# Optimization experiments

Hardware: AMD Instinct MI355X
Metric: run time of the kernel (lower is better)

## Reference

```python
import jax, jax.numpy as jnp
import numpy as np

EPS_LEN = 1e-20
EPS_DENOM = 1e-6


def _dot(a, b):
    return jnp.sum(a * b, axis=-1, keepdims=True)


def _safe_normalize(x):
    return x / jnp.sqrt(jnp.maximum(_dot(x, x), EPS_LEN))


def _auto_normals(positions, faces):
    i0, i1, i2 = faces[:, 0], faces[:, 1], faces[:, 2]
    v0 = positions[i0]
    v1 = positions[i1]
    v2 = positions[i2]
    face_normals = jnp.cross(v1 - v0, v2 - v0)  # [F,3]
    v_nrm = jnp.zeros_like(positions)
    v_nrm = v_nrm.at[i0].add(face_normals)
    v_nrm = v_nrm.at[i1].add(face_normals)
    v_nrm = v_nrm.at[i2].add(face_normals)
    default = jnp.array([0.0, 0.0, 1.0], dtype=positions.dtype)
    v_nrm = jnp.where(_dot(v_nrm, v_nrm) > EPS_LEN, v_nrm, default)
    return _safe_normalize(v_nrm)


def _compute_tangents(positions, normals, faces, texcoords, uv_faces):
    pos = [positions[faces[:, i]] for i in range(3)]
    tex = [texcoords[uv_faces[:, i]] for i in range(3)]
    uve1 = tex[1] - tex[0]
    uve2 = tex[2] - tex[0]
    pe1 = pos[1] - pos[0]
    pe2 = pos[2] - pos[0]
    nom = pe1 * uve2[..., 1:2] - pe2 * uve1[..., 1:2]  # [F,3]
    denom = uve1[..., 0:1] * uve2[..., 1:2] - uve1[..., 1:2] * uve2[..., 0:1]
    denom = jnp.where(denom > 0.0,
                      jnp.maximum(denom, EPS_DENOM),
                      jnp.minimum(denom, -EPS_DENOM))
    tang = nom / denom  # [F,3]
    tangents = jnp.zeros_like(normals)
    for i in range(3):
        tangents = tangents.at[faces[:, i]].add(tang)
    tangents = _safe_normalize(tangents)
    tangents = _safe_normalize(tangents - _dot(tangents, normals) * normals)
    return tangents


def setup_inputs() -> dict:
    key = jax.random.key(0)
    k1, k2, k3, k4 = jax.random.split(key, 4)
    V, T, F = 2_000_000, 2_200_000, 4_000_000
    positions = jax.random.normal(k1, (V, 3), dtype=jnp.float32)
    faces = jax.random.randint(k2, (F, 3), 0, V, dtype=jnp.int32)
    texcoords = jax.random.uniform(k3, (T, 2), dtype=jnp.float32)
    uv_faces = jax.random.randint(k4, (F, 3), 0, T, dtype=jnp.int32)
    return {"positions": positions, "faces": faces,
            "texcoords": texcoords, "uv_faces": uv_faces}


def reference(positions, faces, texcoords, uv_faces):
    normals = _auto_normals(positions, faces)
    tangents = _compute_tangents(positions, normals, faces, texcoords, uv_faces)
    return jnp.stack([normals, tangents])  # [2, V, 3]
```

## Files before the change

### kernel.cpp

```cpp
#include <hip/hip_runtime.h>

#define EPS_LEN   1e-20f
#define EPS_DENOM 1e-6f

#define CB_LOG   13
#define CB       (1 << CB_LOG)
#define QLOG     11
#define QSIZE    (1 << QLOG)
#define CAP_C    57344
#define FST      6
#define BLKA     1024
#define MAXB     256

__global__ __launch_bounds__(BLKA)
void vg_face_bin(const float* __restrict__ pos, const int* __restrict__ faces,
                 const float* __restrict__ tex, const int* __restrict__ uvf,
                 float* __restrict__ face_data,
                 unsigned* __restrict__ ef, unsigned short* __restrict__ ev,
                 int* __restrict__ cursors, int* __restrict__ validw,
                 float* __restrict__ nacc, float* __restrict__ tacc,
                 int F, int NBC)
{
    __shared__ int h[MAXB], sc[MAXB], loff[MAXB], lfill[MAXB], gbase[MAXB];
    __shared__ unsigned       sface[3 * BLKA];
    __shared__ unsigned short svloc[3 * BLKA];
    __shared__ unsigned char  sbuck[3 * BLKA];

    const int t = threadIdx.x;
    const int f = blockIdx.x * BLKA + t;

    if (t < MAXB) { h[t] = 0; lfill[t] = 0; }
    for (int i = t; i < 3 * BLKA; i += BLKA) sbuck[i] = 0xFF;
    __syncthreads();

    const bool on = (f < F);
    int i0 = 0, i1 = 0, i2 = 0;
    float nx = 0, ny = 0, nz = 0, txv = 0, tyv = 0, tzv = 0;

    if (on) {
        i0 = faces[3 * f + 0]; i1 = faces[3 * f + 1]; i2 = faces[3 * f + 2];

        const float p0x = pos[3*i0+0], p0y = pos[3*i0+1], p0z = pos[3*i0+2];
        const float p1x = pos[3*i1+0], p1y = pos[3*i1+1], p1z = pos[3*i1+2];
        const float p2x = pos[3*i2+0], p2y = pos[3*i2+1], p2z = pos[3*i2+2];

        const float e1x = p1x - p0x, e1y = p1y - p0y, e1z = p1z - p0z;
        const float e2x = p2x - p0x, e2y = p2y - p0y, e2z = p2z - p0z;

        nx = e1y * e2z - e1z * e2y;
        ny = e1z * e2x - e1x * e2z;
        nz = e1x * e2y - e1y * e2x;

        const int t0 = uvf[3 * f + 0];
        const int t1 = uvf[3 * f + 1];
        const int t2 = uvf[3 * f + 2];

        const float u0x = tex[2*t0+0], u0y = tex[2*t0+1];
        const float u1x = tex[2*t1+0], u1y = tex[2*t1+1];
        const float u2x = tex[2*t2+0], u2y = tex[2*t2+1];

        const float d1x = u1x - u0x, d1y = u1y - u0y;
        const float d2x = u2x - u0x, d2y = u2y - u0y;

        float denom = d1x * d2y - d1y * d2x;
        denom = (denom > 0.0f) ? fmaxf(denom, EPS_DENOM) : fminf(denom, -EPS_DENOM);
        const float inv = 1.0f / denom;

        txv = (e1x * d2y - e2x * d1y) * inv;
        tyv = (e1y * d2y - e2y * d1y) * inv;
        tzv = (e1z * d2y - e2z * d1y) * inv;

        float* fd = &face_data[(size_t)f * FST];
        reinterpret_cast<float2*>(fd)[0] = make_float2(nx, ny);
        reinterpret_cast<float2*>(fd)[1] = make_float2(nz, txv);
        reinterpret_cast<float2*>(fd)[2] = make_float2(tyv, tzv);

        atomicAdd(&h[i0 >> CB_LOG], 1);
        atomicAdd(&h[i1 >> CB_LOG], 1);
        atomicAdd(&h[i2 >> CB_LOG], 1);
    }
    __syncthreads();

    if (t < MAXB) sc[t] = h[t];
    __syncthreads();
    for (int d = 1; d < MAXB; d <<= 1) {
        int v2 = 0;
        if (t < MAXB) v2 = sc[t] + ((t >= d) ? sc[t - d] : 0);
        __syncthreads();
        if (t < MAXB) sc[t] = v2;
        __syncthreads();
    }
    if (t < MAXB) {
        loff[t] = sc[t] - h[t];
        const int cnt = h[t];
        int gb = -1;
        if (t < NBC && cnt > 0) {
            gb = atomicAdd(&cursors[t], cnt);
            if (gb + cnt <= CAP_C) atomicMax(&validw[t], gb + cnt);
            else gb = -1;
        }
        gbase[t] = gb;
    }
    __syncthreads();

    if (on) {
        const int vi[3] = { i0, i1, i2 };
#pragma unroll
        for (int c = 0; c < 3; ++c) {
            const int v = vi[c];
            const int b = v >> CB_LOG;
            if (gbase[b] >= 0) {
                const int slot = atomicAdd(&lfill[b], 1);
                const int p = loff[b] + slot;
                sface[p] = (unsigned)f;
                svloc[p] = (unsigned short)(v & (CB - 1));
                sbuck[p] = (unsigned char)b;
            } else {
                atomicAdd(&nacc[3*v+0], nx);
                atomicAdd(&nacc[3*v+1], ny);
                atomicAdd(&nacc[3*v+2], nz);
                atomicAdd(&tacc[3*v+0], txv);
                atomicAdd(&tacc[3*v+1], tyv);
                atomicAdd(&tacc[3*v+2], tzv);
            }
        }
    }
    __syncthreads();

    for (int i = t; i < 3 * BLKA; i += BLKA) {
        const unsigned b = sbuck[i];
        if (b != 0xFFu) {
            const int g = gbase[b] + (i - loff[b]);
            const size_t base = (size_t)b * CAP_C;
            ef[base + g] = sface[i];
            ev[base + g] = svloc[i];
        }
    }
}

__global__ __launch_bounds__(BLKA)
void vg_bucket_reduce(const float* __restrict__ face_data,
                      const unsigned* __restrict__ ef,
                      const unsigned short* __restrict__ ev,
                      const int* __restrict__ validw,
                      float* __restrict__ nacc, float* __restrict__ tacc,
                      int V)
{
    __shared__ float acc[QSIZE * 6];
    const int b = blockIdx.x;
    const int t = threadIdx.x;
    int count = validw[b];
    if (count > CAP_C) count = CAP_C;
    const size_t ebase = (size_t)b * CAP_C;
    const int vbase = b << CB_LOG;

    for (int q = 0; q < 4; ++q) {
        for (int i = t; i < QSIZE * 6; i += BLKA) acc[i] = 0.0f;
        __syncthreads();

        for (int e = t; e < count; e += BLKA) {
            const int vloc = (int)ev[ebase + e];
            if ((vloc >> QLOG) == q) {
                const unsigned f = ef[ebase + e];
                const float* fd = &face_data[(size_t)f * FST];
                const float2 a0 = reinterpret_cast<const float2*>(fd)[0];
                const float2 a1 = reinterpret_cast<const float2*>(fd)[1];
                const float2 a2 = reinterpret_cast<const float2*>(fd)[2];
                float* a = &acc[(vloc & (QSIZE - 1)) * 6];
                atomicAdd(a + 0, a0.x);
                atomicAdd(a + 1, a0.y);
                atomicAdd(a + 2, a1.x);
                atomicAdd(a + 3, a1.y);
                atomicAdd(a + 4, a2.x);
                atomicAdd(a + 5, a2.y);
            }
        }
        __syncthreads();

        for (int i = t; i < QSIZE; i += BLKA) {
            const int v = vbase + (q << QLOG) + i;
            if (v < V) {
                float nx = nacc[3*v+0] + acc[i*6+0];
                float ny = nacc[3*v+1] + acc[i*6+1];
                float nz = nacc[3*v+2] + acc[i*6+2];
                float tx = tacc[3*v+0] + acc[i*6+3];
                float ty = tacc[3*v+1] + acc[i*6+4];
                float tz = tacc[3*v+2] + acc[i*6+5];

                const float nd = nx*nx + ny*ny + nz*nz;
                if (nd > EPS_LEN) {
                    const float invn = 1.0f / sqrtf(nd);
                    nx *= invn; ny *= invn; nz *= invn;
                } else {
                    nx = 0.0f; ny = 0.0f; nz = 1.0f;
                }

                const float td = tx*tx + ty*ty + tz*tz;
                const float invt = 1.0f / sqrtf(fmaxf(td, EPS_LEN));
                tx *= invt; ty *= invt; tz *= invt;

                const float dp = tx*nx + ty*ny + tz*nz;
                tx -= dp * nx; ty -= dp * ny; tz -= dp * nz;

                const float td2 = tx*tx + ty*ty + tz*tz;
                const float invt2 = 1.0f / sqrtf(fmaxf(td2, EPS_LEN));
                tx *= invt2; ty *= invt2; tz *= invt2;

                nacc[3*v+0] = nx; nacc[3*v+1] = ny; nacc[3*v+2] = nz;
                tacc[3*v+0] = tx; tacc[3*v+1] = ty; tacc[3*v+2] = tz;
            }
        }
        __syncthreads();
    }
}

__global__ void vg_face_kernel(const float* __restrict__ pos,
                               const int*   __restrict__ faces,
                               const float* __restrict__ tex,
                               const int*   __restrict__ uvf,
                               float* __restrict__ nacc,
                               float* __restrict__ tacc,
                               int F) {
    int f = blockIdx.x * blockDim.x + threadIdx.x;
    if (f >= F) return;

    const int i0 = faces[3*f+0], i1 = faces[3*f+1], i2 = faces[3*f+2];

    const float p0x = pos[3*i0+0], p0y = pos[3*i0+1], p0z = pos[3*i0+2];
    const float p1x = pos[3*i1+0], p1y = pos[3*i1+1], p1z = pos[3*i1+2];
    const float p2x = pos[3*i2+0], p2y = pos[3*i2+1], p2z = pos[3*i2+2];

    const float e1x = p1x - p0x, e1y = p1y - p0y, e1z = p1z - p0z;
    const float e2x = p2x - p0x, e2y = p2y - p0y, e2z = p2z - p0z;

    const float nx = e1y*e2z - e1z*e2y;
    const float ny = e1z*e2x - e1x*e2z;
    const float nz = e1x*e2y - e1y*e2x;

    const int t0 = uvf[3*f+0], t1 = uvf[3*f+1], t2 = uvf[3*f+2];

    const float u0x = tex[2*t0+0], u0y = tex[2*t0+1];
    const float u1x = tex[2*t1+0], u1y = tex[2*t1+1];
    const float u2x = tex[2*t2+0], u2y = tex[2*t2+1];

    const float d1x = u1x - u0x, d1y = u1y - u0y;
    const float d2x = u2x - u0x, d2y = u2y - u0y;

    float denom = d1x * d2y - d1y * d2x;
    denom = (denom > 0.0f) ? fmaxf(denom, EPS_DENOM) : fminf(denom, -EPS_DENOM);
    const float inv = 1.0f / denom;

    const float tx = (e1x*d2y - e2x*d1y) * inv;
    const float ty = (e1y*d2y - e2y*d1y) * inv;
    const float tz = (e1z*d2y - e2z*d1y) * inv;

    atomicAdd(&nacc[3*i0+0], nx); atomicAdd(&nacc[3*i0+1], ny); atomicAdd(&nacc[3*i0+2], nz);
    atomicAdd(&nacc[3*i1+0], nx); atomicAdd(&nacc[3*i1+1], ny); atomicAdd(&nacc[3*i1+2], nz);
    atomicAdd(&nacc[3*i2+0], nx); atomicAdd(&nacc[3*i2+1], ny); atomicAdd(&nacc[3*i2+2], nz);
    atomicAdd(&tacc[3*i0+0], tx); atomicAdd(&tacc[3*i0+1], ty); atomicAdd(&tacc[3*i0+2], tz);
    atomicAdd(&tacc[3*i1+0], tx); atomicAdd(&tacc[3*i1+1], ty); atomicAdd(&tacc[3*i1+2], tz);
    atomicAdd(&tacc[3*i2+0], tx); atomicAdd(&tacc[3*i2+1], ty); atomicAdd(&tacc[3*i2+2], tz);
}

__global__ void vg_finalize_kernel(float* __restrict__ nacc,
                                   float* __restrict__ tacc,
                                   int V) {
    int v = blockIdx.x * blockDim.x + threadIdx.x;
    if (v >= V) return;

    float nx = nacc[3*v+0], ny = nacc[3*v+1], nz = nacc[3*v+2];
    float nd = nx*nx + ny*ny + nz*nz;
    if (nd > EPS_LEN) {
        const float invn = 1.0f / sqrtf(nd);
        nx *= invn; ny *= invn; nz *= invn;
    } else {
        nx = 0.0f; ny = 0.0f; nz = 1.0f;
    }

    float tx = tacc[3*v+0], ty = tacc[3*v+1], tz = tacc[3*v+2];
    float td = tx*tx + ty*ty + tz*tz;
    float invt = 1.0f / sqrtf(fmaxf(td, EPS_LEN));
    tx *= invt; ty *= invt; tz *= invt;
    const float dp = tx*nx + ty*ny + tz*nz;
    tx -= dp*nx; ty -= dp*ny; tz -= dp*nz;
    float td2 = tx*tx + ty*ty + tz*tz;
    float invt2 = 1.0f / sqrtf(fmaxf(td2, EPS_LEN));
    tx *= invt2; ty *= invt2; tz *= invt2;

    nacc[3*v+0] = nx; nacc[3*v+1] = ny; nacc[3*v+2] = nz;
    tacc[3*v+0] = tx; tacc[3*v+1] = ty; tacc[3*v+2] = tz;
}

extern "C" void kernel_launch(void* const* d_in, const int* in_sizes, int n_in,
                              void* d_out, int out_size, void* d_ws, size_t ws_size,
                              hipStream_t stream) {
    const float* pos   = (const float*)d_in[0];
    const int*   faces = (const int*)  d_in[1];
    const float* tex   = (const float*)d_in[2];
    const int*   uvf   = (const int*)  d_in[3];

    const int V = in_sizes[0] / 3;
    const int F = in_sizes[1] / 3;

    float* out  = (float*)d_out;
    float* nacc = out;
    float* tacc = out + (size_t)3 * V;

    const int NBC = (V + CB - 1) >> CB_LOG;

    const size_t face_bytes = ((size_t)F * FST * sizeof(float) + 255) & ~(size_t)255;
    const size_t ef_bytes   = ((size_t)NBC * CAP_C * sizeof(unsigned) + 255) & ~(size_t)255;
    const size_t ev_bytes   = ((size_t)NBC * CAP_C * sizeof(unsigned short) + 255) & ~(size_t)255;
    const size_t cur_bytes  = (size_t)NBC * sizeof(int);
    const size_t need = face_bytes + ef_bytes + ev_bytes + 2 * cur_bytes + 256;

    hipMemsetAsync(d_out, 0, (size_t)out_size * sizeof(float), stream);

    if (ws_size < need || NBC > 255 || F >= (1 << 22)) {
        const int BLK = 256;
        vg_face_kernel<<<(F + BLK - 1) / BLK, BLK, 0, stream>>>(pos, faces, tex, uvf,
                                                                nacc, tacc, F);
        vg_finalize_kernel<<<(V + BLK - 1) / BLK, BLK, 0, stream>>>(nacc, tacc, V);
        return;
    }

    char* ws = (char*)d_ws;
    float*          face_data = (float*)ws;
    unsigned*       ef        = (unsigned*)(ws + face_bytes);
    unsigned short* ev        = (unsigned short*)(ws + face_bytes + ef_bytes);
    int*            cursors   = (int*)(ws + face_bytes + ef_bytes + ev_bytes);
    int*            validw    = cursors + NBC;

    hipMemsetAsync(cursors, 0, 2 * cur_bytes, stream);

    vg_face_bin<<<(F + BLKA - 1) / BLKA, BLKA, 0, stream>>>(
        pos, faces, tex, uvf, face_data, ef, ev, cursors, validw, nacc, tacc, F, NBC);

    vg_bucket_reduce<<<NBC, BLKA, 0, stream>>>(
        face_data, ef, ev, validw, nacc, tacc, V);
}
```

Baseline: 937.3 us.

## Bin face payloads directly per vertex bucket instead of face indices

The binning kernel now writes the face normal and tangent values straight into per-bucket payload arrays, in place of a face index that the reduce kernel then uses for a random gather from face_data. The new reduce kernel streams those payloads sequentially and accumulates a whole 8192-vertex bucket in shared memory in one pass, finalizing normals and then tangents. The goal is to replace scattered gathers and the four-pass quarter loop with coalesced reads. In exchange, binned entries grow from 6 to 26 bytes each, so workspace use and write traffic rise, and the per-bucket capacity shrinks, sending more overflow entries to global atomics.

```diff
diff --git a/kernel.cpp b/kernel.cpp
--- a/kernel.cpp
+++ b/kernel.cpp
@@ -5,24 +5,28 @@
 
 #define CB_LOG   13
 #define CB       (1 << CB_LOG)
+#define BLKA     1024
+#define MAXB     256
+#define CAP1     50176
+#define CAP2     57344
+#define FST      6
 #define QLOG     11
 #define QSIZE    (1 << QLOG)
-#define CAP_C    57344
-#define FST      6
-#define BLKA     1024
-#define MAXB     256
+#define VPT      (CB / BLKA)
 
 __global__ __launch_bounds__(BLKA)
-void vg_face_bin(const float* __restrict__ pos, const int* __restrict__ faces,
-                 const float* __restrict__ tex, const int* __restrict__ uvf,
-                 float* __restrict__ face_data,
-                 unsigned* __restrict__ ef, unsigned short* __restrict__ ev,
-                 int* __restrict__ cursors, int* __restrict__ validw,
-                 float* __restrict__ nacc, float* __restrict__ tacc,
-                 int F, int NBC)
+void vg_face_bin_pay(const float* __restrict__ pos, const int* __restrict__ faces,
+                     const float* __restrict__ tex, const int* __restrict__ uvf,
+                     float* __restrict__ en, float* __restrict__ et,
+                     unsigned short* __restrict__ ev,
+                     int* __restrict__ cursors, int* __restrict__ validw,
+                     float* __restrict__ nacc, float* __restrict__ tacc,
+                     int F, int NBC)
 {
     __shared__ int h[MAXB], sc[MAXB], loff[MAXB], lfill[MAXB], gbase[MAXB];
-    __shared__ unsigned       sface[3 * BLKA];
+    __shared__ float spnx[BLKA], spny[BLKA], spnz[BLKA];
+    __shared__ float sptx[BLKA], spty[BLKA], sptz[BLKA];
+    __shared__ unsigned short sfl[3 * BLKA];
     __shared__ unsigned short svloc[3 * BLKA];
     __shared__ unsigned char  sbuck[3 * BLKA];
 
@@ -70,10 +74,8 @@
         tyv = (e1y * d2y - e2y * d1y) * inv;
         tzv = (e1z * d2y - e2z * d1y) * inv;
 
-        float* fd = &face_data[(size_t)f * FST];
-        reinterpret_cast<float2*>(fd)[0] = make_float2(nx, ny);
-        reinterpret_cast<float2*>(fd)[1] = make_float2(nz, txv);
-        reinterpret_cast<float2*>(fd)[2] = make_float2(tyv, tzv);
+        spnx[t] = nx;  spny[t] = ny;  spnz[t] = nz;
+        sptx[t] = txv; spty[t] = tyv; sptz[t] = tzv;
 
         atomicAdd(&h[i0 >> CB_LOG], 1);
         atomicAdd(&h[i1 >> CB_LOG], 1);
@@ -96,7 +98,228 @@
         int gb = -1;
         if (t < NBC && cnt > 0) {
             gb = atomicAdd(&cursors[t], cnt);
-            if (gb + cnt <= CAP_C) atomicMax(&validw[t], gb + cnt);
+            if (gb + cnt <= CAP1) atomicMax(&validw[t], gb + cnt);
+            else gb = -1;
+        }
+        gbase[t] = gb;
+    }
+    __syncthreads();
+
+    if (on) {
+        const int vi[3] = { i0, i1, i2 };
+#pragma unroll
+        for (int c = 0; c < 3; ++c) {
+            const int v = vi[c];
+            const int b = v >> CB_LOG;
+            if (gbase[b] >= 0) {
+                const int slot = atomicAdd(&lfill[b], 1);
+                const int p = loff[b] + slot;
+                sfl[p]   = (unsigned short)t;
+                svloc[p] = (unsigned short)(v & (CB - 1));
+                sbuck[p] = (unsigned char)b;
+            } else {
+                atomicAdd(&nacc[3*v+0], nx);
+                atomicAdd(&nacc[3*v+1], ny);
+                atomicAdd(&nacc[3*v+2], nz);
+                atomicAdd(&tacc[3*v+0], txv);
+                atomicAdd(&tacc[3*v+1], tyv);
+                atomicAdd(&tacc[3*v+2], tzv);
+            }
+        }
+    }
+    __syncthreads();
+
+    for (int i = t; i < 3 * BLKA; i += BLKA) {
+        const unsigned b = sbuck[i];
+        if (b != 0xFFu) {
+            const int g = gbase[b] + (i - loff[b]);
+            const size_t s = (size_t)b * CAP1 + g;
+            const int fl = sfl[i];
+            float* pn = &en[s * 3];
+            pn[0] = spnx[fl]; pn[1] = spny[fl]; pn[2] = spnz[fl];
+            float* pt = &et[s * 3];
+            pt[0] = sptx[fl]; pt[1] = spty[fl]; pt[2] = sptz[fl];
+            ev[s] = svloc[i];
+        }
+    }
+}
+
+__global__ __launch_bounds__(BLKA)
+void vg_reduce_pay(const float* __restrict__ en, const float* __restrict__ et,
+                   const unsigned short* __restrict__ ev,
+                   const int* __restrict__ validw,
+                   float* __restrict__ nacc, float* __restrict__ tacc,
+                   int V)
+{
+    __shared__ float acc[CB * 3];
+    const int b = blockIdx.x;
+    const int t = threadIdx.x;
+    int count = validw[b];
+    if (count > CAP1) count = CAP1;
+    const size_t ebase = (size_t)b * CAP1;
+    const int vbase = b << CB_LOG;
+
+    float nreg[VPT][3];
+
+    for (int i = t; i < CB * 3; i += BLKA) acc[i] = 0.0f;
+    __syncthreads();
+
+    for (int e = t; e < count; e += BLKA) {
+        const int vloc = (int)ev[ebase + e];
+        const float* p = &en[(ebase + e) * 3];
+        float* a = &acc[vloc * 3];
+        atomicAdd(a + 0, p[0]);
+        atomicAdd(a + 1, p[1]);
+        atomicAdd(a + 2, p[2]);
+    }
+    __syncthreads();
+
+#pragma unroll
+    for (int k = 0; k < VPT; ++k) {
+        const int i = t + k * BLKA;
+        const int v = vbase + i;
+        float nx = 0.0f, ny = 0.0f, nz = 1.0f;
+        if (v < V) {
+            nx = nacc[3*v+0] + acc[3*i+0];
+            ny = nacc[3*v+1] + acc[3*i+1];
+            nz = nacc[3*v+2] + acc[3*i+2];
+            const float nd = nx*nx + ny*ny + nz*nz;
+            if (nd > EPS_LEN) {
+                const float invn = 1.0f / sqrtf(nd);
+                nx *= invn; ny *= invn; nz *= invn;
+            } else {
+                nx = 0.0f; ny = 0.0f; nz = 1.0f;
+            }
+            nacc[3*v+0] = nx; nacc[3*v+1] = ny; nacc[3*v+2] = nz;
+        }
+        nreg[k][0] = nx; nreg[k][1] = ny; nreg[k][2] = nz;
+    }
+    __syncthreads();
+
+    for (int i = t; i < CB * 3; i += BLKA) acc[i] = 0.0f;
+    __syncthreads();
+
+    for (int e = t; e < count; e += BLKA) {
+        const int vloc = (int)ev[ebase + e];
+        const float* p = &et[(ebase + e) * 3];
+        float* a = &acc[vloc * 3];
+        atomicAdd(a + 0, p[0]);
+        atomicAdd(a + 1, p[1]);
+        atomicAdd(a + 2, p[2]);
+    }
+    __syncthreads();
+
+#pragma unroll
+    for (int k = 0; k < VPT; ++k) {
+        const int i = t + k * BLKA;
+        const int v = vbase + i;
+        if (v < V) {
+            float tx = tacc[3*v+0] + acc[3*i+0];
+            float ty = tacc[3*v+1] + acc[3*i+1];
+            float tz = tacc[3*v+2] + acc[3*i+2];
+            const float nx = nreg[k][0], ny = nreg[k][1], nz = nreg[k][2];
+
+            const float td = tx*tx + ty*ty + tz*tz;
+            const float invt = 1.0f / sqrtf(fmaxf(td, EPS_LEN));
+            tx *= invt; ty *= invt; tz *= invt;
+
+            const float dp = tx*nx + ty*ny + tz*nz;
+            tx -= dp * nx; ty -= dp * ny; tz -= dp * nz;
+
+            const float td2 = tx*tx + ty*ty + tz*tz;
+            const float invt2 = 1.0f / sqrtf(fmaxf(td2, EPS_LEN));
+            tx *= invt2; ty *= invt2; tz *= invt2;
+
+            tacc[3*v+0] = tx; tacc[3*v+1] = ty; tacc[3*v+2] = tz;
+        }
+    }
+}
+
+__global__ __launch_bounds__(BLKA)
+void vg_face_bin3(const float* __restrict__ pos, const int* __restrict__ faces,
+                  const float* __restrict__ tex, const int* __restrict__ uvf,
+                  float* __restrict__ face_data,
+                  unsigned* __restrict__ ef, unsigned short* __restrict__ ev,
+                  int* __restrict__ cursors, int* __restrict__ validw,
+                  float* __restrict__ nacc, float* __restrict__ tacc,
+                  int F, int NBC)
+{
+    __shared__ int h[MAXB], sc[MAXB], loff[MAXB], lfill[MAXB], gbase[MAXB];
+    __shared__ unsigned       sface[3 * BLKA];
+    __shared__ unsigned short svloc[3 * BLKA];
+    __shared__ unsigned char  sbuck[3 * BLKA];
+
+    const int t = threadIdx.x;
+    const int f = blockIdx.x * BLKA + t;
+
+    if (t < MAXB) { h[t] = 0; lfill[t] = 0; }
+    for (int i = t; i < 3 * BLKA; i += BLKA) sbuck[i] = 0xFF;
+    __syncthreads();
+
+    const bool on = (f < F);
+    int i0 = 0, i1 = 0, i2 = 0;
+    float nx = 0, ny = 0, nz = 0, txv = 0, tyv = 0, tzv = 0;
+
+    if (on) {
+        i0 = faces[3 * f + 0]; i1 = faces[3 * f + 1]; i2 = faces[3 * f + 2];
+
+        const float p0x = pos[3*i0+0], p0y = pos[3*i0+1], p0z = pos[3*i0+2];
+        const float p1x = pos[3*i1+0], p1y = pos[3*i1+1], p1z = pos[3*i1+2];
+        const float p2x = pos[3*i2+0], p2y = pos[3*i2+1], p2z = pos[3*i2+2];
+
+        const float e1x = p1x - p0x, e1y = p1y - p0y, e1z = p1z - p0z;
+        const float e2x = p2x - p0x, e2y = p2y - p0y, e2z = p2z - p0z;
+
+        nx = e1y * e2z - e1z * e2y;
+        ny = e1z * e2x - e1x * e2z;
+        nz = e1x * e2y - e1y * e2x;
+
+        const int t0 = uvf[3 * f + 0];
+        const int t1 = uvf[3 * f + 1];
+        const int t2 = uvf[3 * f + 2];
+
+        const float u0x = tex[2*t0+0], u0y = tex[2*t0+1];
+        const float u1x = tex[2*t1+0], u1y = tex[2*t1+1];
+        const float u2x = tex[2*t2+0], u2y = tex[2*t2+1];
+
+        const float d1x = u1x - u0x, d1y = u1y - u0y;
+        const float d2x = u2x - u0x, d2y = u2y - u0y;
+
+        float denom = d1x * d2y - d1y * d2x;
+        denom = (denom > 0.0f) ? fmaxf(denom, EPS_DENOM) : fminf(denom, -EPS_DENOM);
+        const float inv = 1.0f / denom;
+
+        txv = (e1x * d2y - e2x * d1y) * inv;
+        tyv = (e1y * d2y - e2y * d1y) * inv;
+        tzv = (e1z * d2y - e2z * d1y) * inv;
+
+        float* fd = &face_data[(size_t)f * FST];
+        reinterpret_cast<float2*>(fd)[0] = make_float2(nx, ny);
+        reinterpret_cast<float2*>(fd)[1] = make_float2(nz, txv);
+        reinterpret_cast<float2*>(fd)[2] = make_float2(tyv, tzv);
+
+        atomicAdd(&h[i0 >> CB_LOG], 1);
+        atomicAdd(&h[i1 >> CB_LOG], 1);
+        atomicAdd(&h[i2 >> CB_LOG], 1);
+    }
+    __syncthreads();
+
+    if (t < MAXB) sc[t] = h[t];
+    __syncthreads();
+    for (int d = 1; d < MAXB; d <<= 1) {
+        int v2 = 0;
+        if (t < MAXB) v2 = sc[t] + ((t >= d) ? sc[t - d] : 0);
+        __syncthreads();
+        if (t < MAXB) sc[t] = v2;
+        __syncthreads();
+    }
+    if (t < MAXB) {
+        loff[t] = sc[t] - h[t];
+        const int cnt = h[t];
+        int gb = -1;
+        if (t < NBC && cnt > 0) {
+            gb = atomicAdd(&cursors[t], cnt);
+            if (gb + cnt <= CAP2) atomicMax(&validw[t], gb + cnt);
             else gb = -1;
         }
         gbase[t] = gb;
@@ -131,7 +354,7 @@
         const unsigned b = sbuck[i];
         if (b != 0xFFu) {
             const int g = gbase[b] + (i - loff[b]);
-            const size_t base = (size_t)b * CAP_C;
+            const size_t base = (size_t)b * CAP2;
             ef[base + g] = sface[i];
             ev[base + g] = svloc[i];
         }
@@ -139,19 +362,19 @@
 }
 
 __global__ __launch_bounds__(BLKA)
-void vg_bucket_reduce(const float* __restrict__ face_data,
-                      const unsigned* __restrict__ ef,
-                      const unsigned short* __restrict__ ev,
-                      const int* __restrict__ validw,
-                      float* __restrict__ nacc, float* __restrict__ tacc,
-                      int V)
+void vg_bucket_reduce3(const float* __restrict__ face_data,
+                       const unsigned* __restrict__ ef,
+                       const unsigned short* __restrict__ ev,
+                       const int* __restrict__ validw,
+                       float* __restrict__ nacc, float* __restrict__ tacc,
+                       int V)
 {
     __shared__ float acc[QSIZE * 6];
     const int b = blockIdx.x;
     const int t = threadIdx.x;
     int count = validw[b];
-    if (count > CAP_C) count = CAP_C;
-    const size_t ebase = (size_t)b * CAP_C;
+    if (count > CAP2) count = CAP2;
+    const size_t ebase = (size_t)b * CAP2;
     const int vbase = b << CB_LOG;
 
     for (int q = 0; q < 4; ++q) {
@@ -307,35 +530,59 @@
     float* tacc = out + (size_t)3 * V;
 
     const int NBC = (V + CB - 1) >> CB_LOG;
-
-    const size_t face_bytes = ((size_t)F * FST * sizeof(float) + 255) & ~(size_t)255;
-    const size_t ef_bytes   = ((size_t)NBC * CAP_C * sizeof(unsigned) + 255) & ~(size_t)255;
-    const size_t ev_bytes   = ((size_t)NBC * CAP_C * sizeof(unsigned short) + 255) & ~(size_t)255;
-    const size_t cur_bytes  = (size_t)NBC * sizeof(int);
-    const size_t need = face_bytes + ef_bytes + ev_bytes + 2 * cur_bytes + 256;
+    const size_t cur_b = (size_t)NBC * sizeof(int);
 
     hipMemsetAsync(d_out, 0, (size_t)out_size * sizeof(float), stream);
 
-    if (ws_size < need || NBC > 255 || F >= (1 << 22)) {
-        const int BLK = 256;
-        vg_face_kernel<<<(F + BLK - 1) / BLK, BLK, 0, stream>>>(pos, faces, tex, uvf,
-                                                                nacc, tacc, F);
-        vg_finalize_kernel<<<(V + BLK - 1) / BLK, BLK, 0, stream>>>(nacc, tacc, V);
+    const size_t NE1   = (size_t)NBC * CAP1;
+    const size_t en_b  = (NE1 * 12 + 255) & ~(size_t)255;
+    const size_t et_b  = (NE1 * 12 + 255) & ~(size_t)255;
+    const size_t ev1_b = (NE1 * 2 + 255) & ~(size_t)255;
+    const size_t need1 = en_b + et_b + ev1_b + 2 * cur_b + 256;
+
+    if (ws_size >= need1 && NBC <= 255) {
+        char* ws = (char*)d_ws;
+        float*          en  = (float*)ws;                ws += en_b;
+        float*          et  = (float*)ws;                ws += et_b;
+        unsigned short* ev  = (unsigned short*)ws;       ws += ev1_b;
+        int*            cursors = (int*)ws;
+        int*            validw  = cursors + NBC;
+
+        hipMemsetAsync(cursors, 0, 2 * cur_b, stream);
+
+        vg_face_bin_pay<<<(F + BLKA - 1) / BLKA, BLKA, 0, stream>>>(
+            pos, faces, tex, uvf, en, et, ev, cursors, validw, nacc, tacc, F, NBC);
+        vg_reduce_pay<<<NBC, BLKA, 0, stream>>>(
+            en, et, ev, validw, nacc, tacc, V);
         return;
     }
 
-    char* ws = (char*)d_ws;
-    float*          face_data = (float*)ws;
-    unsigned*       ef        = (unsigned*)(ws + face_bytes);
-    unsigned short* ev        = (unsigned short*)(ws + face_bytes + ef_bytes);
-    int*            cursors   = (int*)(ws + face_bytes + ef_bytes + ev_bytes);
-    int*            validw    = cursors + NBC;
-
-    hipMemsetAsync(cursors, 0, 2 * cur_bytes, stream);
-
-    vg_face_bin<<<(F + BLKA - 1) / BLKA, BLKA, 0, stream>>>(
-        pos, faces, tex, uvf, face_data, ef, ev, cursors, validw, nacc, tacc, F, NBC);
-
-    vg_bucket_reduce<<<NBC, BLKA, 0, stream>>>(
-        face_data, ef, ev, validw, nacc, tacc, V);
-}
+    const size_t NE2    = (size_t)NBC * CAP2;
+    const size_t face_b = ((size_t)F * FST * sizeof(float) + 255) & ~(size_t)255;
+    const size_t ef_b   = (NE2 * 4 + 255) & ~(size_t)255;
+    const size_t ev2_b  = (NE2 * 2 + 255) & ~(size_t)255;
+    const size_t need2  = face_b + ef_b + ev2_b + 2 * cur_b + 256;
+
+    if (ws_size >= need2 && NBC <= 255 && F < (1 << 22)) {
+        char* ws = (char*)d_ws;
+        float*          face_data = (float*)ws;          ws += face_b;
+        unsigned*       ef        = (unsigned*)ws;       ws += ef_b;
+        unsigned short* ev        = (unsigned short*)ws; ws += ev2_b;
+        int*            cursors   = (int*)ws;
+        int*            validw    = cursors + NBC;
+
+        hipMemsetAsync(cursors, 0, 2 * cur_b, stream);
+
+        vg_face_bin3<<<(F + BLKA - 1) / BLKA, BLKA, 0, stream>>>(
+            pos, faces, tex, uvf, face_data, ef, ev, cursors, validw,
+            nacc, tacc, F, NBC);
+        vg_bucket_reduce3<<<NBC, BLKA, 0, stream>>>(
+            face_data, ef, ev, validw, nacc, tacc, V);
+        return;
+    }
+
+    const int BLK = 256;
+    vg_face_kernel<<<(F + BLK - 1) / BLK, BLK, 0, stream>>>(pos, faces, tex, uvf,
+                                                            nacc, tacc, F);
+    vg_finalize_kernel<<<(V + BLK - 1) / BLK, BLK, 0, stream>>>(nacc, tacc, V);
+}
```

Result: no change. 936.1 us (-0.1%).
